# Kernel optimization log

Measured on AMD Instinct MI355X. Metric: run time of the kernel, lower is better.

The kernel has to match this reference:

```python
import jax, jax.numpy as jnp
import numpy as np
import math

B = 512          # graphs per batch
NP = 200         # nodes per graph
E_PER = 2000     # edges per graph
V = 50000        # item vocab
EMB = 9
HID = 128
RATIO = 0.8
K1 = math.ceil(RATIO * NP)   # 160
K2 = math.ceil(RATIO * K1)   # 128
K3 = math.ceil(RATIO * K2)   # 103


def sage_conv(x, src, dst, valid, n, w_neigh, w_root, b):
    # PyG SAGEConv: lin_l(mean_{j->i} x_j) + lin_r(x_i) + bias
    msg = x[src] * valid[:, None]                      # [E, C]
    seg = jnp.where(valid > 0, dst, n)                 # invalid edges -> dummy segment
    s = jax.ops.segment_sum(msg, seg, num_segments=n + 1)[:n]
    cnt = jax.ops.segment_sum(valid, seg, num_segments=n + 1)[:n]
    mean = s / jnp.maximum(cnt, 1.0)[:, None]
    return mean @ w_neigh.T + x @ w_root.T + b


def topk_pool(x, src, dst, valid, np_cur, k, p):
    # TopKPooling: score = tanh(x.p/||p||); keep top-k per graph; x *= score
    n = x.shape[0]
    score = jnp.tanh((x @ p) / jnp.linalg.norm(p))
    topv, topi = jax.lax.top_k(score.reshape(B, np_cur), k)   # [B, k]
    kept = (jnp.arange(B)[:, None] * np_cur + topi).reshape(-1)
    n_new = B * k
    x_new = x[kept] * topv.reshape(-1)[:, None]
    mapping = jnp.full((n,), -1, dtype=jnp.int32).at[kept].set(
        jnp.arange(n_new, dtype=jnp.int32))
    ns, nd = mapping[src], mapping[dst]
    valid_new = valid * ((ns >= 0) & (nd >= 0)).astype(valid.dtype)
    return x_new, jnp.maximum(ns, 0), jnp.maximum(nd, 0), valid_new


def global_pool(x, k):
    # cat([global_max_pool, global_mean_pool]) with uniform graph size k
    xr = x.reshape(B, k, -1)
    return jnp.concatenate([xr.max(axis=1), xr.mean(axis=1)], axis=1)


def setup_inputs() -> dict:
    key = jax.random.key(0)
    ks = jax.random.split(key, 24)
    # block-structured intra-graph edges
    s = jax.random.randint(ks[0], (B, E_PER), 0, NP)
    d = jax.random.randint(ks[1], (B, E_PER), 0, NP)
    off = (jnp.arange(B) * NP)[:, None]
    edge_index = jnp.stack([(s + off).reshape(-1), (d + off).reshape(-1)]).astype(jnp.int32)
    node_ids = jax.random.randint(ks[2], (B * NP, 1), 0, V)
    batch = jnp.repeat(jnp.arange(B), NP)
    sc = 0.1
    p = {
        'emb': jax.random.normal(ks[3], (V, EMB)) * sc,
        'w1n': jax.random.normal(ks[4], (HID, EMB)) * sc,
        'w1r': jax.random.normal(ks[5], (HID, EMB)) * sc,
        'b1': jnp.zeros((HID,)),
        'w2n': jax.random.normal(ks[6], (HID, HID)) * sc,
        'w2r': jax.random.normal(ks[7], (HID, HID)) * sc,
        'b2': jnp.zeros((HID,)),
        'w3n': jax.random.normal(ks[8], (HID, HID)) * sc,
        'w3r': jax.random.normal(ks[9], (HID, HID)) * sc,
        'b3': jnp.zeros((HID,)),
        'p1': jax.random.normal(ks[10], (HID,)) * sc,
        'p2': jax.random.normal(ks[11], (HID,)) * sc,
        'p3': jax.random.normal(ks[12], (HID,)) * sc,
        'lw1': jax.random.normal(ks[13], (HID, 2 * HID)) * sc,
        'lb1': jnp.zeros((HID,)),
        'lw2': jax.random.normal(ks[14], (64, HID)) * sc,
        'lb2': jnp.zeros((64,)),
        'lw3': jax.random.normal(ks[15], (1, 64)) * sc,
        'lb3': jnp.zeros((1,)),
    }
    return {'node_ids': node_ids, 'edge_index': edge_index, 'batch': batch, **p}


def reference(node_ids, edge_index, batch, emb, w1n, w1r, b1, w2n, w2r, b2,
              w3n, w3r, b3, p1, p2, p3, lw1, lb1, lw2, lb2, lw3, lb3):
    src, dst = edge_index[0], edge_index[1]
    valid = jnp.ones(src.shape[0], dtype=jnp.float32)
    x = emb[node_ids[:, 0]]                                  # [N, 9]
    x = jax.nn.relu(sage_conv(x, src, dst, valid, B * NP, w1n, w1r, b1))
    x, src, dst, valid = topk_pool(x, src, dst, valid, NP, K1, p1)
    x1 = global_pool(x, K1)
    x = jax.nn.relu(sage_conv(x, src, dst, valid, B * K1, w2n, w2r, b2))
    x, src, dst, valid = topk_pool(x, src, dst, valid, K1, K2, p2)
    x2 = global_pool(x, K2)
    x = jax.nn.relu(sage_conv(x, src, dst, valid, B * K2, w3n, w3r, b3))
    x, src, dst, valid = topk_pool(x, src, dst, valid, K2, K3, p3)
    x3 = global_pool(x, K3)
    h = x1 + x2 + x3                                         # [B, 256]
    h = jax.nn.relu(h @ lw1.T + lb1)
    h = jax.nn.relu(h @ lw2.T + lb2)
    return jax.nn.sigmoid(h @ lw3.T + lb3)[:, 0]             # [B]
```

## Files before the change

kernel.cpp:

```cpp
#include <hip/hip_runtime.h>
#include <math.h>

constexpr int B    = 512;
constexpr int NPG  = 200;
constexpr int EPER = 2000;
constexpr int EMB  = 9;
constexpr int HID  = 128;
constexpr int K1   = 160;
constexpr int K2   = 128;
constexpr int K3   = 103;
constexpr int N0   = B * NPG;
constexpr int N1   = B * K1;
constexpr int N2   = B * K2;
constexpr int E    = B * EPER;

__global__ __launch_bounds__(256) void k_stage1(
        const int* __restrict__ node_ids,
        const float* __restrict__ emb,
        const int* __restrict__ es, const int* __restrict__ ed,
        const float* __restrict__ w1n, const float* __restrict__ w1r,
        const float* __restrict__ b1, const float* __restrict__ p1,
        float* __restrict__ xout,
        int* __restrict__ mapping,
        float* __restrict__ gout) {
    const int g = blockIdx.x, tid = threadIdx.x;
    __shared__ float x0L[NPG * EMB];
    __shared__ float mnL[NPG * EMB];
    __shared__ int   idsL[NPG];
    __shared__ int   deg[256];
    __shared__ int   off2[257];
    __shared__ int   cur[256];
    __shared__ int   csr[EPER];
    __shared__ float sc[NPG];
    __shared__ int   pos[NPG];
    __shared__ float redM[4 * 128], redS[4 * 128];

    if (tid < NPG) idsL[tid] = node_ids[g * NPG + tid];
    deg[tid] = 0;
    __syncthreads();
    for (int i = tid; i < NPG * EMB; i += 256) {
        int n = i / EMB, j = i - n * EMB;
        x0L[i] = emb[(size_t)idsL[n] * EMB + j];
    }
    const int ebase = g * EPER, nbase = g * NPG;
    int lsrc[8], ldst[8];
    #pragma unroll
    for (int q = 0; q < 8; q++) {
        int e = tid + q * 256;
        lsrc[q] = es[ebase + e] - nbase;
        ldst[q] = ed[ebase + e] - nbase;
        atomicAdd(&deg[ldst[q]], 1);
    }
    __syncthreads();
    cur[tid] = deg[tid];
    __syncthreads();
    #pragma unroll
    for (int d = 1; d < 256; d <<= 1) {
        int t = (tid >= d) ? cur[tid - d] : 0;
        __syncthreads();
        cur[tid] += t;
        __syncthreads();
    }
    if (tid == 0) off2[0] = 0;
    off2[tid + 1] = cur[tid];
    __syncthreads();
    cur[tid] = off2[tid];
    __syncthreads();
    #pragma unroll
    for (int q = 0; q < 8; q++) {
        int slot = atomicAdd(&cur[ldst[q]], 1);
        csr[slot] = lsrc[q];
    }
    __syncthreads();
    if (tid < NPG) {
        int bg = off2[tid], en = off2[tid + 1];
        float a[EMB];
        #pragma unroll
        for (int j = 0; j < EMB; j++) a[j] = 0.f;
        for (int t = bg; t < en; t++) {
            int s = csr[t];
            #pragma unroll
            for (int j = 0; j < EMB; j++) a[j] += x0L[s * EMB + j];
        }
        float inv = 1.f / (float)((en - bg) > 1 ? (en - bg) : 1);
        #pragma unroll
        for (int j = 0; j < EMB; j++) mnL[tid * EMB + j] = a[j] * inv;
    }
    const int lane = tid & 63, wv = tid >> 6;
    float pl0 = p1[lane], pl1 = p1[64 + lane];
    float pp = pl0 * pl0 + pl1 * pl1;
    #pragma unroll
    for (int o = 32; o >= 1; o >>= 1) pp += __shfl_xor(pp, o, 64);
    float nrm = sqrtf(pp);
    float wn0[EMB], wn1[EMB], wr0[EMB], wr1[EMB];
    #pragma unroll
    for (int j = 0; j < EMB; j++) {
        wn0[j] = w1n[lane * EMB + j];
        wn1[j] = w1n[(lane + 64) * EMB + j];
        wr0[j] = w1r[lane * EMB + j];
        wr1[j] = w1r[(lane + 64) * EMB + j];
    }
    float bb0 = b1[lane], bb1 = b1[64 + lane];
    __syncthreads();
    for (int i = wv; i < NPG; i += 4) {
        float c0 = bb0, c1 = bb1;
        #pragma unroll
        for (int j = 0; j < EMB; j++) {
            float m = mnL[i * EMB + j];
            float x = x0L[i * EMB + j];
            c0 += m * wn0[j] + x * wr0[j];
            c1 += m * wn1[j] + x * wr1[j];
        }
        c0 = fmaxf(c0, 0.f);
        c1 = fmaxf(c1, 0.f);
        float d = c0 * pl0 + c1 * pl1;
        #pragma unroll
        for (int o = 32; o >= 1; o >>= 1) d += __shfl_xor(d, o, 64);
        if (lane == 0) sc[i] = tanhf(d / nrm);
    }
    __syncthreads();
    if (tid < NPG) {
        float scv = sc[tid];
        int rank = 0;
        for (int j = 0; j < NPG; j++) {
            float o = sc[j];
            rank += (o > scv) || (o == scv && j < tid);
        }
        bool keep = rank < K1;
        pos[tid] = keep ? rank : -1;
        mapping[g * NPG + tid] = keep ? (g * K1 + rank) : -1;
    }
    __syncthreads();
    float pm0 = -INFINITY, pm1 = -INFINITY, ps0 = 0.f, ps1 = 0.f;
    for (int i = wv; i < NPG; i += 4) {
        int r = pos[i];
        if (r < 0) continue;
        float c0 = bb0, c1 = bb1;
        #pragma unroll
        for (int j = 0; j < EMB; j++) {
            float m = mnL[i * EMB + j];
            float x = x0L[i * EMB + j];
            c0 += m * wn0[j] + x * wr0[j];
            c1 += m * wn1[j] + x * wr1[j];
        }
        float s = sc[i];
        float v0 = fmaxf(c0, 0.f) * s;
        float v1 = fmaxf(c1, 0.f) * s;
        long rowp = (long)(g * K1 + r) * HID;
        xout[rowp + lane] = v0;
        xout[rowp + 64 + lane] = v1;
        pm0 = fmaxf(pm0, v0); ps0 += v0;
        pm1 = fmaxf(pm1, v1); ps1 += v1;
    }
    redM[wv * 128 + lane] = pm0;      redS[wv * 128 + lane] = ps0;
    redM[wv * 128 + 64 + lane] = pm1; redS[wv * 128 + 64 + lane] = ps1;
    __syncthreads();
    if (tid < 128) {
        float mx = redM[tid], sm = redS[tid];
        #pragma unroll
        for (int w2 = 1; w2 < 4; w2++) {
            mx = fmaxf(mx, redM[w2 * 128 + tid]);
            sm += redS[w2 * 128 + tid];
        }
        gout[g * 256 + tid] = mx;
        gout[g * 256 + 128 + tid] = sm / (float)K1;
    }
}

template <int MROWS, int KKEEP, int NTHR, int MINW>
__global__ __launch_bounds__(NTHR, MINW) void k_stage23(
        const float* __restrict__ xin,
        const int* __restrict__ es, const int* __restrict__ ed,
        const int* __restrict__ map1,
        const int* __restrict__ map2,
        const float* __restrict__ wn, const float* __restrict__ wr,
        const float* __restrict__ bb, const float* __restrict__ p,
        float* __restrict__ xout,
        int* __restrict__ mapout,
        float* __restrict__ gout) {
    constexpr int TRM = MROWS / 8;
    __shared__ float xY[MROWS * 132];
    __shared__ float Bw[2 * 32 * 132];
    __shared__ int   csr[EPER];
    __shared__ int   deg[256], scanb[256], off2[257], cur[256];
    __shared__ float sc[MROWS];
    __shared__ int   pos[MROWS];
    __shared__ float nrmL;

    const int tid = threadIdx.x;
    const int g = blockIdx.x;
    const long row0 = (long)g * MROWS;
    const int tc = tid & 31, tr = tid >> 5;

    for (int i = tid; i < MROWS * 32; i += NTHR) {
        int r = i >> 5, c = (i & 31) * 4;
        *(float4*)&xY[r * 132 + c] =
            *(const float4*)(xin + (row0 + r) * HID + c);
    }
    if (tid < 256) deg[tid] = 0;
    __syncthreads();
    const int ebase = g * EPER, nbase = g * MROWS;
    for (int e = tid; e < EPER; e += NTHR) {
        int a = map1[es[ebase + e]];
        int b = map1[ed[ebase + e]];
        if (map2) {
            a = (a >= 0) ? map2[a] : -1;
            b = (b >= 0) ? map2[b] : -1;
        }
        if (a >= 0 && b >= 0) atomicAdd(&deg[b - nbase], 1);
    }
    __syncthreads();
    if (tid < 256) scanb[tid] = deg[tid];
    __syncthreads();
    #pragma unroll
    for (int d = 1; d < 256; d <<= 1) {
        int t = (tid < 256 && tid >= d) ? scanb[tid - d] : 0;
        __syncthreads();
        if (tid < 256) scanb[tid] += t;
        __syncthreads();
    }
    if (tid == 0) off2[0] = 0;
    if (tid < 256) off2[tid + 1] = scanb[tid];
    __syncthreads();
    if (tid < 256) cur[tid] = off2[tid];
    __syncthreads();
    for (int e = tid; e < EPER; e += NTHR) {
        int a = map1[es[ebase + e]];
        int b = map1[ed[ebase + e]];
        if (map2) {
            a = (a >= 0) ? map2[a] : -1;
            b = (b >= 0) ? map2[b] : -1;
        }
        if (a >= 0 && b >= 0) {
            int slot = atomicAdd(&cur[b - nbase], 1);
            csr[slot] = a - nbase;
        }
    }
    if (tid < 64) {
        float a = p[tid], b2 = p[64 + tid];
        float pp = a * a + b2 * b2;
        #pragma unroll
        for (int o = 32; o >= 1; o >>= 1) pp += __shfl_xor(pp, o, 64);
        if (tid == 0) nrmL = sqrtf(pp);
    }
    __syncthreads();

    float accY[8][4], accZ[8][4];
    #pragma unroll
    for (int r = 0; r < 8; r++)
        #pragma unroll
        for (int c = 0; c < 4; c++) { accY[r][c] = 0.f; accZ[r][c] = 0.f; }

    const int sr = tid >> 3, sc4 = (tid & 7) * 4;
    const bool stager = (sr < 64);
    const float* wsrc0 = (sr < 32) ? wn : wr;
    const int wrow = (sr < 32) ? sr : sr - 32;
    float* Bmine = Bw + ((sr < 32) ? 0 : 32 * 132);
    float4 bvv[4];
    if (stager) {
        #pragma unroll
        for (int i = 0; i < 4; i++)
            bvv[i] = *(const float4*)(wsrc0 + (size_t)(wrow + i * 32) * HID + sc4);
    }
    for (int ch = 0; ch < 4; ch++) {
        if (stager) {
            #pragma unroll
            for (int i = 0; i < 4; i++) {
                int r = wrow + i * 32;
                Bmine[(sc4 + 0) * 132 + r] = bvv[i].x;
                Bmine[(sc4 + 1) * 132 + r] = bvv[i].y;
                Bmine[(sc4 + 2) * 132 + r] = bvv[i].z;
                Bmine[(sc4 + 3) * 132 + r] = bvv[i].w;
            }
        }
        __syncthreads();
        if (ch + 1 < 4 && stager) {
            #pragma unroll
            for (int i = 0; i < 4; i++)
                bvv[i] = *(const float4*)(wsrc0 + (size_t)(wrow + i * 32) * HID
                                          + (ch + 1) * 32 + sc4);
        }
        for (int kq = 0; kq < 8; kq++) {
            float4 af[8];
            #pragma unroll
            for (int rr = 0; rr < 8; rr++)
                af[rr] = *(const float4*)&xY[(tr * 8 + rr) * 132 + ch * 32 + kq * 4];
            #pragma unroll
            for (int kk = 0; kk < 4; kk++) {
                int k = kq * 4 + kk;
                float4 bn = *(const float4*)&Bw[k * 132 + tc * 4];
                float4 br = *(const float4*)&Bw[32 * 132 + k * 132 + tc * 4];
                #pragma unroll
                for (int rr = 0; rr < 8; rr++) {
                    float a = (kk == 0) ? af[rr].x : (kk == 1) ? af[rr].y
                             : (kk == 2) ? af[rr].z : af[rr].w;
                    accY[rr][0] += a * bn.x; accY[rr][1] += a * bn.y;
                    accY[rr][2] += a * bn.z; accY[rr][3] += a * bn.w;
                    accZ[rr][0] += a * br.x; accZ[rr][1] += a * br.y;
                    accZ[rr][2] += a * br.z; accZ[rr][3] += a * br.w;
                }
            }
        }
        __syncthreads();
    }

    #pragma unroll
    for (int rr = 0; rr < 8; rr++) {
        float4 yv = {accY[rr][0], accY[rr][1], accY[rr][2], accY[rr][3]};
        *(float4*)&xY[(tr * 8 + rr) * 132 + tc * 4] = yv;
    }
    __syncthreads();

    float bias[4], pv[4];
    #pragma unroll
    for (int c = 0; c < 4; c++) {
        bias[c] = bb[tc * 4 + c];
        pv[c]   = p[tc * 4 + c];
    }
    float outv[8][4];
    #pragma unroll
    for (int rr = 0; rr < 8; rr++) {
        int m = tr * 8 + rr;
        int bg = off2[m], en = off2[m + 1];
        float s0 = 0.f, s1 = 0.f, s2 = 0.f, s3 = 0.f;
        for (int t = bg; t < en; t++) {
            float4 yv = *(const float4*)&xY[csr[t] * 132 + tc * 4];
            s0 += yv.x; s1 += yv.y; s2 += yv.z; s3 += yv.w;
        }
        float inv = 1.f / (float)((en - bg) > 1 ? (en - bg) : 1);
        outv[rr][0] = fmaxf(s0 * inv + accZ[rr][0] + bias[0], 0.f);
        outv[rr][1] = fmaxf(s1 * inv + accZ[rr][1] + bias[1], 0.f);
        outv[rr][2] = fmaxf(s2 * inv + accZ[rr][2] + bias[2], 0.f);
        outv[rr][3] = fmaxf(s3 * inv + accZ[rr][3] + bias[3], 0.f);
    }

    float* scpart = Bw;
    #pragma unroll
    for (int rr = 0; rr < 8; rr++) {
        float sp = outv[rr][0] * pv[0] + outv[rr][1] * pv[1]
                 + outv[rr][2] * pv[2] + outv[rr][3] * pv[3];
        scpart[(tr * 8 + rr) * 32 + tc] = sp;
    }
    __syncthreads();
    if (tid < MROWS) {
        float sum = 0.f;
        #pragma unroll
        for (int t = 0; t < 32; t++) sum += scpart[tid * 32 + t];
        sc[tid] = tanhf(sum / nrmL);
    }
    __syncthreads();
    if (tid < MROWS) {
        float scv = sc[tid];
        int rank = 0;
        for (int j = 0; j < MROWS; j++) {
            float o = sc[j];
            rank += (o > scv) || (o == scv && j < tid);
        }
        bool keep = rank < KKEEP;
        pos[tid] = keep ? rank : -1;
        if (mapout) mapout[g * MROWS + tid] = keep ? (g * KKEEP + rank) : -1;
    }
    __syncthreads();
    float cm[4], cs[4];
    #pragma unroll
    for (int c = 0; c < 4; c++) { cm[c] = -INFINITY; cs[c] = 0.f; }
    #pragma unroll
    for (int rr = 0; rr < 8; rr++) {
        int m = tr * 8 + rr;
        int r = pos[m];
        if (r < 0) continue;
        float sv = sc[m];
        float v0 = outv[rr][0] * sv, v1 = outv[rr][1] * sv;
        float v2 = outv[rr][2] * sv, v3 = outv[rr][3] * sv;
        cm[0] = fmaxf(cm[0], v0); cs[0] += v0;
        cm[1] = fmaxf(cm[1], v1); cs[1] += v1;
        cm[2] = fmaxf(cm[2], v2); cs[2] += v2;
        cm[3] = fmaxf(cm[3], v3); cs[3] += v3;
        if (xout) {
            float4 o0 = {v0, v1, v2, v3};
            *(float4*)(xout + ((long)g * KKEEP + r) * HID + tc * 4) = o0;
        }
    }
    float* redM = Bw;
    float* redS = Bw + TRM * 128;
    #pragma unroll
    for (int c = 0; c < 4; c++) {
        redM[tr * 128 + tc * 4 + c] = cm[c];
        redS[tr * 128 + tc * 4 + c] = cs[c];
    }
    __syncthreads();
    if (tid < 128) {
        float mx = redM[tid], sm = redS[tid];
        #pragma unroll 4
        for (int t = 1; t < TRM; t++) {
            mx = fmaxf(mx, redM[t * 128 + tid]);
            sm += redS[t * 128 + tid];
        }
        gout[g * 256 + tid] = mx;
        gout[g * 256 + 128 + tid] = sm / (float)KKEEP;
    }
}

__global__ __launch_bounds__(128) void k_mlp(const float* __restrict__ g1, const float* __restrict__ g2,
                      const float* __restrict__ g3,
                      const float* __restrict__ lw1, const float* __restrict__ lb1,
                      const float* __restrict__ lw2, const float* __restrict__ lb2,
                      const float* __restrict__ lw3, const float* __restrict__ lb3,
                      float* __restrict__ out) {
    int g = blockIdx.x, t = threadIdx.x;
    __shared__ float h0[256];
    __shared__ float h1[128];
    __shared__ float h2r[64];
    h0[t]       = g1[g * 256 + t] + g2[g * 256 + t] + g3[g * 256 + t];
    h0[t + 128] = g1[g * 256 + 128 + t] + g2[g * 256 + 128 + t] + g3[g * 256 + 128 + t];
    __syncthreads();
    float a = lb1[t];
    #pragma unroll 4
    for (int j = 0; j < 256; j++) a += h0[j] * lw1[t * 256 + j];
    h1[t] = fmaxf(a, 0.f);
    __syncthreads();
    if (t < 64) {
        float a2 = lb2[t];
        #pragma unroll 4
        for (int j = 0; j < 128; j++) a2 += h1[j] * lw2[t * 128 + j];
        h2r[t] = fmaxf(a2, 0.f) * lw3[t];
    }
    __syncthreads();
    if (t == 0) {
        float s = 0.f;
        for (int j = 0; j < 64; j++) s += h2r[j];
        s += lb3[0];
        out[g] = 1.f / (1.f + expf(-s));
    }
}

extern "C" void kernel_launch(void* const* d_in, const int* in_sizes, int n_in,
                              void* d_out, int out_size, void* d_ws, size_t ws_size,
                              hipStream_t stream) {
    const int*   node_ids = (const int*)d_in[0];
    const int*   ei   = (const int*)d_in[1];
    const float* emb  = (const float*)d_in[3];
    const float* w1n  = (const float*)d_in[4];
    const float* w1r  = (const float*)d_in[5];
    const float* b1   = (const float*)d_in[6];
    const float* w2n  = (const float*)d_in[7];
    const float* w2r  = (const float*)d_in[8];
    const float* b2   = (const float*)d_in[9];
    const float* w3n  = (const float*)d_in[10];
    const float* w3r  = (const float*)d_in[11];
    const float* b3   = (const float*)d_in[12];
    const float* p1   = (const float*)d_in[13];
    const float* p2   = (const float*)d_in[14];
    const float* p3   = (const float*)d_in[15];
    const float* lw1  = (const float*)d_in[16];
    const float* lb1  = (const float*)d_in[17];
    const float* lw2  = (const float*)d_in[18];
    const float* lb2  = (const float*)d_in[19];
    const float* lw3  = (const float*)d_in[20];
    const float* lb3  = (const float*)d_in[21];
    float* out = (float*)d_out;

    float* ws  = (float*)d_ws;
    float* D   = ws;
    float* D2  = D + (size_t)N1 * HID;
    float* g1  = D2 + (size_t)N2 * HID;
    float* g2  = g1 + B * 2 * HID;
    float* g3  = g2 + B * 2 * HID;
    int* map1  = (int*)(g3 + B * 2 * HID);
    int* map2  = map1 + N0;

    k_stage1<<<B, 256, 0, stream>>>(node_ids, emb, ei, ei + E,
                                    w1n, w1r, b1, p1, D, map1, g1);

    k_stage23<K1, K2, 640, 3><<<B, 640, 0, stream>>>(
        D, ei, ei + E, map1, nullptr, w2n, w2r, b2, p2, D2, map2, g2);

    k_stage23<K2, K3, 512, 2><<<B, 512, 0, stream>>>(
        D2, ei, ei + E, map1, map2, w3n, w3r, b3, p3, nullptr, nullptr, g3);

    k_mlp<<<B, 128, 0, stream>>>(g1, g2, g3, lw1, lb1, lw2, lb2, lw3, lb3, out);
}
```

Measured before the change: 379.1 us.

## Fuse all three conv/pool stages into one per-graph kernel

Merges stage1 and both stage2/3 kernels into a single 640-thread block per graph that keeps pooled node features in shared memory between stages. Edge remapping uses local shared-memory position arrays instead of global mapping tables. This removes the global write and re-read of the intermediate feature matrices and mapping arrays, plus two kernel launches. In exchange it uses a larger shared-memory footprint and runs stage 1 with a 640-thread block, which may limit occupancy.

```diff
diff --git a/kernel.cpp b/kernel.cpp
--- a/kernel.cpp
+++ b/kernel.cpp
@@ -9,395 +9,555 @@
 constexpr int K1   = 160;
 constexpr int K2   = 128;
 constexpr int K3   = 103;
-constexpr int N0   = B * NPG;
-constexpr int N1   = B * K1;
-constexpr int N2   = B * K2;
 constexpr int E    = B * EPER;
 
-__global__ __launch_bounds__(256) void k_stage1(
+__global__ __launch_bounds__(640, 2) void k_fused(
         const int* __restrict__ node_ids,
         const float* __restrict__ emb,
         const int* __restrict__ es, const int* __restrict__ ed,
         const float* __restrict__ w1n, const float* __restrict__ w1r,
         const float* __restrict__ b1, const float* __restrict__ p1,
-        float* __restrict__ xout,
-        int* __restrict__ mapping,
-        float* __restrict__ gout) {
+        const float* __restrict__ w2n, const float* __restrict__ w2r,
+        const float* __restrict__ b2, const float* __restrict__ p2,
+        const float* __restrict__ w3n, const float* __restrict__ w3r,
+        const float* __restrict__ b3, const float* __restrict__ p3,
+        float* __restrict__ g1, float* __restrict__ g2,
+        float* __restrict__ g3) {
     const int g = blockIdx.x, tid = threadIdx.x;
-    __shared__ float x0L[NPG * EMB];
-    __shared__ float mnL[NPG * EMB];
-    __shared__ int   idsL[NPG];
-    __shared__ int   deg[256];
-    __shared__ int   off2[257];
-    __shared__ int   cur[256];
-    __shared__ int   csr[EPER];
-    __shared__ float sc[NPG];
-    __shared__ int   pos[NPG];
-    __shared__ float redM[4 * 128], redS[4 * 128];
-
-    if (tid < NPG) idsL[tid] = node_ids[g * NPG + tid];
-    deg[tid] = 0;
-    __syncthreads();
-    for (int i = tid; i < NPG * EMB; i += 256) {
-        int n = i / EMB, j = i - n * EMB;
-        x0L[i] = emb[(size_t)idsL[n] * EMB + j];
-    }
-    const int ebase = g * EPER, nbase = g * NPG;
-    int lsrc[8], ldst[8];
-    #pragma unroll
-    for (int q = 0; q < 8; q++) {
-        int e = tid + q * 256;
-        lsrc[q] = es[ebase + e] - nbase;
-        ldst[q] = ed[ebase + e] - nbase;
-        atomicAdd(&deg[ldst[q]], 1);
-    }
-    __syncthreads();
-    cur[tid] = deg[tid];
-    __syncthreads();
-    #pragma unroll
-    for (int d = 1; d < 256; d <<= 1) {
-        int t = (tid >= d) ? cur[tid - d] : 0;
-        __syncthreads();
-        cur[tid] += t;
-        __syncthreads();
-    }
-    if (tid == 0) off2[0] = 0;
-    off2[tid + 1] = cur[tid];
-    __syncthreads();
-    cur[tid] = off2[tid];
-    __syncthreads();
-    #pragma unroll
-    for (int q = 0; q < 8; q++) {
-        int slot = atomicAdd(&cur[ldst[q]], 1);
-        csr[slot] = lsrc[q];
-    }
-    __syncthreads();
-    if (tid < NPG) {
-        int bg = off2[tid], en = off2[tid + 1];
-        float a[EMB];
-        #pragma unroll
-        for (int j = 0; j < EMB; j++) a[j] = 0.f;
-        for (int t = bg; t < en; t++) {
-            int s = csr[t];
-            #pragma unroll
-            for (int j = 0; j < EMB; j++) a[j] += x0L[s * EMB + j];
-        }
-        float inv = 1.f / (float)((en - bg) > 1 ? (en - bg) : 1);
-        #pragma unroll
-        for (int j = 0; j < EMB; j++) mnL[tid * EMB + j] = a[j] * inv;
-    }
     const int lane = tid & 63, wv = tid >> 6;
-    float pl0 = p1[lane], pl1 = p1[64 + lane];
-    float pp = pl0 * pl0 + pl1 * pl1;
-    #pragma unroll
-    for (int o = 32; o >= 1; o >>= 1) pp += __shfl_xor(pp, o, 64);
-    float nrm = sqrtf(pp);
-    float wn0[EMB], wn1[EMB], wr0[EMB], wr1[EMB];
-    #pragma unroll
-    for (int j = 0; j < EMB; j++) {
-        wn0[j] = w1n[lane * EMB + j];
-        wn1[j] = w1n[(lane + 64) * EMB + j];
-        wr0[j] = w1r[lane * EMB + j];
-        wr1[j] = w1r[(lane + 64) * EMB + j];
-    }
-    float bb0 = b1[lane], bb1 = b1[64 + lane];
-    __syncthreads();
-    for (int i = wv; i < NPG; i += 4) {
-        float c0 = bb0, c1 = bb1;
-        #pragma unroll
-        for (int j = 0; j < EMB; j++) {
-            float m = mnL[i * EMB + j];
-            float x = x0L[i * EMB + j];
-            c0 += m * wn0[j] + x * wr0[j];
-            c1 += m * wn1[j] + x * wr1[j];
-        }
-        c0 = fmaxf(c0, 0.f);
-        c1 = fmaxf(c1, 0.f);
-        float d = c0 * pl0 + c1 * pl1;
-        #pragma unroll
-        for (int o = 32; o >= 1; o >>= 1) d += __shfl_xor(d, o, 64);
-        if (lane == 0) sc[i] = tanhf(d / nrm);
-    }
-    __syncthreads();
-    if (tid < NPG) {
-        float scv = sc[tid];
-        int rank = 0;
-        for (int j = 0; j < NPG; j++) {
-            float o = sc[j];
-            rank += (o > scv) || (o == scv && j < tid);
-        }
-        bool keep = rank < K1;
-        pos[tid] = keep ? rank : -1;
-        mapping[g * NPG + tid] = keep ? (g * K1 + rank) : -1;
-    }
-    __syncthreads();
-    float pm0 = -INFINITY, pm1 = -INFINITY, ps0 = 0.f, ps1 = 0.f;
-    for (int i = wv; i < NPG; i += 4) {
-        int r = pos[i];
-        if (r < 0) continue;
-        float c0 = bb0, c1 = bb1;
-        #pragma unroll
-        for (int j = 0; j < EMB; j++) {
-            float m = mnL[i * EMB + j];
-            float x = x0L[i * EMB + j];
-            c0 += m * wn0[j] + x * wr0[j];
-            c1 += m * wn1[j] + x * wr1[j];
-        }
-        float s = sc[i];
-        float v0 = fmaxf(c0, 0.f) * s;
-        float v1 = fmaxf(c1, 0.f) * s;
-        long rowp = (long)(g * K1 + r) * HID;
-        xout[rowp + lane] = v0;
-        xout[rowp + 64 + lane] = v1;
-        pm0 = fmaxf(pm0, v0); ps0 += v0;
-        pm1 = fmaxf(pm1, v1); ps1 += v1;
-    }
-    redM[wv * 128 + lane] = pm0;      redS[wv * 128 + lane] = ps0;
-    redM[wv * 128 + 64 + lane] = pm1; redS[wv * 128 + 64 + lane] = ps1;
-    __syncthreads();
-    if (tid < 128) {
-        float mx = redM[tid], sm = redS[tid];
-        #pragma unroll
-        for (int w2 = 1; w2 < 4; w2++) {
-            mx = fmaxf(mx, redM[w2 * 128 + tid]);
-            sm += redS[w2 * 128 + tid];
-        }
-        gout[g * 256 + tid] = mx;
-        gout[g * 256 + 128 + tid] = sm / (float)K1;
-    }
-}
-
-template <int MROWS, int KKEEP, int NTHR, int MINW>
-__global__ __launch_bounds__(NTHR, MINW) void k_stage23(
-        const float* __restrict__ xin,
-        const int* __restrict__ es, const int* __restrict__ ed,
-        const int* __restrict__ map1,
-        const int* __restrict__ map2,
-        const float* __restrict__ wn, const float* __restrict__ wr,
-        const float* __restrict__ bb, const float* __restrict__ p,
-        float* __restrict__ xout,
-        int* __restrict__ mapout,
-        float* __restrict__ gout) {
-    constexpr int TRM = MROWS / 8;
-    __shared__ float xY[MROWS * 132];
-    __shared__ float Bw[2 * 32 * 132];
+
+    __shared__ float xY[K1 * 132];
+    __shared__ float S[2 * 32 * 132];
     __shared__ int   csr[EPER];
     __shared__ int   deg[256], scanb[256], off2[257], cur[256];
-    __shared__ float sc[MROWS];
-    __shared__ int   pos[MROWS];
-    __shared__ float nrmL;
-
-    const int tid = threadIdx.x;
-    const int g = blockIdx.x;
-    const long row0 = (long)g * MROWS;
-    const int tc = tid & 31, tr = tid >> 5;
-
-    for (int i = tid; i < MROWS * 32; i += NTHR) {
-        int r = i >> 5, c = (i & 31) * 4;
-        *(float4*)&xY[r * 132 + c] =
-            *(const float4*)(xin + (row0 + r) * HID + c);
+    __shared__ int   idsL[NPG];
+    __shared__ float sc[NPG];
+    __shared__ int   pos1[NPG], pos2[K1];
+
+    const int eb = g * EPER, nb0 = g * NPG;
+
+    {
+        float* x0L  = S;
+        float* mnL  = S + 1800;
+        float* redA = S + 3600;
+        if (tid < NPG) idsL[tid] = node_ids[g * NPG + tid];
+        if (tid < 256) deg[tid] = 0;
+        __syncthreads();
+        for (int i = tid; i < NPG * EMB; i += 640) {
+            int n = i / EMB, j = i - n * EMB;
+            x0L[i] = emb[(size_t)idsL[n] * EMB + j];
+        }
+        for (int e = tid; e < EPER; e += 640)
+            atomicAdd(&deg[ed[eb + e] - nb0], 1);
+        __syncthreads();
+        if (tid < 256) scanb[tid] = deg[tid];
+        __syncthreads();
+        #pragma unroll
+        for (int d = 1; d < 256; d <<= 1) {
+            int t = (tid < 256 && tid >= d) ? scanb[tid - d] : 0;
+            __syncthreads();
+            if (tid < 256) scanb[tid] += t;
+            __syncthreads();
+        }
+        if (tid == 0) off2[0] = 0;
+        if (tid < 256) off2[tid + 1] = scanb[tid];
+        __syncthreads();
+        if (tid < 256) cur[tid] = off2[tid];
+        __syncthreads();
+        for (int e = tid; e < EPER; e += 640) {
+            int slot = atomicAdd(&cur[ed[eb + e] - nb0], 1);
+            csr[slot] = es[eb + e] - nb0;
+        }
+        __syncthreads();
+        if (tid < NPG) {
+            int bg = off2[tid], en = off2[tid + 1];
+            float a[EMB];
+            #pragma unroll
+            for (int j = 0; j < EMB; j++) a[j] = 0.f;
+            for (int t = bg; t < en; t++) {
+                int s = csr[t];
+                #pragma unroll
+                for (int j = 0; j < EMB; j++) a[j] += x0L[s * EMB + j];
+            }
+            float inv = 1.f / (float)((en - bg) > 1 ? (en - bg) : 1);
+            #pragma unroll
+            for (int j = 0; j < EMB; j++) mnL[tid * EMB + j] = a[j] * inv;
+        }
+        float pl0 = p1[lane], pl1 = p1[64 + lane];
+        float pp = pl0 * pl0 + pl1 * pl1;
+        #pragma unroll
+        for (int o = 32; o >= 1; o >>= 1) pp += __shfl_xor(pp, o, 64);
+        float nrm = sqrtf(pp);
+        float wn0[EMB], wn1[EMB], wr0[EMB], wr1[EMB];
+        #pragma unroll
+        for (int j = 0; j < EMB; j++) {
+            wn0[j] = w1n[lane * EMB + j];
+            wn1[j] = w1n[(lane + 64) * EMB + j];
+            wr0[j] = w1r[lane * EMB + j];
+            wr1[j] = w1r[(lane + 64) * EMB + j];
+        }
+        float bb0 = b1[lane], bb1 = b1[64 + lane];
+        __syncthreads();
+        for (int i = wv; i < NPG; i += 10) {
+            float c0 = bb0, c1 = bb1;
+            #pragma unroll
+            for (int j = 0; j < EMB; j++) {
+                float m = mnL[i * EMB + j];
+                float x = x0L[i * EMB + j];
+                c0 += m * wn0[j] + x * wr0[j];
+                c1 += m * wn1[j] + x * wr1[j];
+            }
+            c0 = fmaxf(c0, 0.f);
+            c1 = fmaxf(c1, 0.f);
+            float d = c0 * pl0 + c1 * pl1;
+            #pragma unroll
+            for (int o = 32; o >= 1; o >>= 1) d += __shfl_xor(d, o, 64);
+            if (lane == 0) sc[i] = tanhf(d / nrm);
+        }
+        __syncthreads();
+        if (tid < NPG) {
+            float scv = sc[tid];
+            int rank = 0;
+            for (int j = 0; j < NPG; j++) {
+                float o = sc[j];
+                rank += (o > scv) || (o == scv && j < tid);
+            }
+            pos1[tid] = (rank < K1) ? rank : -1;
+        }
+        __syncthreads();
+        float pm0 = -INFINITY, pm1 = -INFINITY, ps0 = 0.f, ps1 = 0.f;
+        for (int i = wv; i < NPG; i += 10) {
+            int r = pos1[i];
+            if (r < 0) continue;
+            float c0 = bb0, c1 = bb1;
+            #pragma unroll
+            for (int j = 0; j < EMB; j++) {
+                float m = mnL[i * EMB + j];
+                float x = x0L[i * EMB + j];
+                c0 += m * wn0[j] + x * wr0[j];
+                c1 += m * wn1[j] + x * wr1[j];
+            }
+            float s = sc[i];
+            float v0 = fmaxf(c0, 0.f) * s;
+            float v1 = fmaxf(c1, 0.f) * s;
+            xY[r * 132 + lane] = v0;
+            xY[r * 132 + 64 + lane] = v1;
+            pm0 = fmaxf(pm0, v0); ps0 += v0;
+            pm1 = fmaxf(pm1, v1); ps1 += v1;
+        }
+        redA[wv * 128 + lane] = pm0;
+        redA[wv * 128 + 64 + lane] = pm1;
+        redA[1280 + wv * 128 + lane] = ps0;
+        redA[1280 + wv * 128 + 64 + lane] = ps1;
+        __syncthreads();
+        if (tid < 128) {
+            float mx = redA[tid], sm = redA[1280 + tid];
+            #pragma unroll
+            for (int w = 1; w < 10; w++) {
+                mx = fmaxf(mx, redA[w * 128 + tid]);
+                sm += redA[1280 + w * 128 + tid];
+            }
+            g1[g * 256 + tid] = mx;
+            g1[g * 256 + 128 + tid] = sm / (float)K1;
+        }
+        __syncthreads();
     }
-    if (tid < 256) deg[tid] = 0;
-    __syncthreads();
-    const int ebase = g * EPER, nbase = g * MROWS;
-    for (int e = tid; e < EPER; e += NTHR) {
-        int a = map1[es[ebase + e]];
-        int b = map1[ed[ebase + e]];
-        if (map2) {
-            a = (a >= 0) ? map2[a] : -1;
-            b = (b >= 0) ? map2[b] : -1;
-        }
-        if (a >= 0 && b >= 0) atomicAdd(&deg[b - nbase], 1);
+
+    {
+        if (tid < 256) deg[tid] = 0;
+        __syncthreads();
+        for (int e = tid; e < EPER; e += 640) {
+            int a = pos1[es[eb + e] - nb0];
+            int b = pos1[ed[eb + e] - nb0];
+            if (a >= 0 && b >= 0) atomicAdd(&deg[b], 1);
+        }
+        __syncthreads();
+        if (tid < 256) scanb[tid] = deg[tid];
+        __syncthreads();
+        #pragma unroll
+        for (int d = 1; d < 256; d <<= 1) {
+            int t = (tid < 256 && tid >= d) ? scanb[tid - d] : 0;
+            __syncthreads();
+            if (tid < 256) scanb[tid] += t;
+            __syncthreads();
+        }
+        if (tid == 0) off2[0] = 0;
+        if (tid < 256) off2[tid + 1] = scanb[tid];
+        __syncthreads();
+        if (tid < 256) cur[tid] = off2[tid];
+        __syncthreads();
+        for (int e = tid; e < EPER; e += 640) {
+            int a = pos1[es[eb + e] - nb0];
+            int b = pos1[ed[eb + e] - nb0];
+            if (a >= 0 && b >= 0) {
+                int slot = atomicAdd(&cur[b], 1);
+                csr[slot] = a;
+            }
+        }
+        __syncthreads();
+
+        const int tc = tid & 31, tr = tid >> 5;
+        float accY[8][4], accZ[8][4];
+        #pragma unroll
+        for (int r = 0; r < 8; r++)
+            #pragma unroll
+            for (int c = 0; c < 4; c++) { accY[r][c] = 0.f; accZ[r][c] = 0.f; }
+
+        const int sr = tid >> 3, sc4 = (tid & 7) * 4;
+        const bool stager = (sr < 64);
+        const float* wsrc0 = (sr < 32) ? w2n : w2r;
+        const int wrow = (sr < 32) ? sr : sr - 32;
+        float* Bmine = S + ((sr < 32) ? 0 : 32 * 132);
+        float4 bvv[4];
+        if (stager) {
+            #pragma unroll
+            for (int i = 0; i < 4; i++)
+                bvv[i] = *(const float4*)(wsrc0 + (size_t)(wrow + i * 32) * HID + sc4);
+        }
+        for (int ch = 0; ch < 4; ch++) {
+            if (stager) {
+                #pragma unroll
+                for (int i = 0; i < 4; i++) {
+                    int r = wrow + i * 32;
+                    Bmine[(sc4 + 0) * 132 + r] = bvv[i].x;
+                    Bmine[(sc4 + 1) * 132 + r] = bvv[i].y;
+                    Bmine[(sc4 + 2) * 132 + r] = bvv[i].z;
+                    Bmine[(sc4 + 3) * 132 + r] = bvv[i].w;
+                }
+            }
+            __syncthreads();
+            if (ch + 1 < 4 && stager) {
+                #pragma unroll
+                for (int i = 0; i < 4; i++)
+                    bvv[i] = *(const float4*)(wsrc0 + (size_t)(wrow + i * 32) * HID
+                                              + (ch + 1) * 32 + sc4);
+            }
+            for (int kq = 0; kq < 8; kq++) {
+                float4 af[8];
+                #pragma unroll
+                for (int rr = 0; rr < 8; rr++)
+                    af[rr] = *(const float4*)&xY[(tr * 8 + rr) * 132 + ch * 32 + kq * 4];
+                #pragma unroll
+                for (int kk = 0; kk < 4; kk++) {
+                    int k = kq * 4 + kk;
+                    float4 bn = *(const float4*)&S[k * 132 + tc * 4];
+                    float4 br = *(const float4*)&S[32 * 132 + k * 132 + tc * 4];
+                    #pragma unroll
+                    for (int rr = 0; rr < 8; rr++) {
+                        float a = (kk == 0) ? af[rr].x : (kk == 1) ? af[rr].y
+                                 : (kk == 2) ? af[rr].z : af[rr].w;
+                        accY[rr][0] += a * bn.x; accY[rr][1] += a * bn.y;
+                        accY[rr][2] += a * bn.z; accY[rr][3] += a * bn.w;
+                        accZ[rr][0] += a * br.x; accZ[rr][1] += a * br.y;
+                        accZ[rr][2] += a * br.z; accZ[rr][3] += a * br.w;
+                    }
+                }
+            }
+            __syncthreads();
+        }
+        #pragma unroll
+        for (int rr = 0; rr < 8; rr++) {
+            float4 yv = {accY[rr][0], accY[rr][1], accY[rr][2], accY[rr][3]};
+            *(float4*)&xY[(tr * 8 + rr) * 132 + tc * 4] = yv;
+        }
+        __syncthreads();
+
+        float bias[4], pv[4];
+        #pragma unroll
+        for (int c = 0; c < 4; c++) {
+            bias[c] = b2[tc * 4 + c];
+            pv[c]   = p2[tc * 4 + c];
+        }
+        float a0 = p2[lane], a1 = p2[64 + lane];
+        float pp = a0 * a0 + a1 * a1;
+        #pragma unroll
+        for (int o = 32; o >= 1; o >>= 1) pp += __shfl_xor(pp, o, 64);
+        float nrm = sqrtf(pp);
+        float outv[8][4];
+        #pragma unroll
+        for (int rr = 0; rr < 8; rr++) {
+            int m = tr * 8 + rr;
+            int bg = off2[m], en = off2[m + 1];
+            float s0 = 0.f, s1 = 0.f, s2 = 0.f, s3 = 0.f;
+            for (int t = bg; t < en; t++) {
+                float4 yv = *(const float4*)&xY[csr[t] * 132 + tc * 4];
+                s0 += yv.x; s1 += yv.y; s2 += yv.z; s3 += yv.w;
+            }
+            float inv = 1.f / (float)((en - bg) > 1 ? (en - bg) : 1);
+            outv[rr][0] = fmaxf(s0 * inv + accZ[rr][0] + bias[0], 0.f);
+            outv[rr][1] = fmaxf(s1 * inv + accZ[rr][1] + bias[1], 0.f);
+            outv[rr][2] = fmaxf(s2 * inv + accZ[rr][2] + bias[2], 0.f);
+            outv[rr][3] = fmaxf(s3 * inv + accZ[rr][3] + bias[3], 0.f);
+        }
+        float* scpart = S;
+        __syncthreads();
+        #pragma unroll
+        for (int rr = 0; rr < 8; rr++) {
+            float sp = outv[rr][0] * pv[0] + outv[rr][1] * pv[1]
+                     + outv[rr][2] * pv[2] + outv[rr][3] * pv[3];
+            scpart[(tr * 8 + rr) * 32 + tc] = sp;
+        }
+        __syncthreads();
+        if (tid < K1) {
+            float sum = 0.f;
+            #pragma unroll
+            for (int t = 0; t < 32; t++) sum += scpart[tid * 32 + t];
+            sc[tid] = tanhf(sum / nrm);
+        }
+        __syncthreads();
+        if (tid < K1) {
+            float scv = sc[tid];
+            int rank = 0;
+            for (int j = 0; j < K1; j++) {
+                float o = sc[j];
+                rank += (o > scv) || (o == scv && j < tid);
+            }
+            pos2[tid] = (rank < K2) ? rank : -1;
+        }
+        __syncthreads();
+        float cm[4], cs[4];
+        #pragma unroll
+        for (int c = 0; c < 4; c++) { cm[c] = -INFINITY; cs[c] = 0.f; }
+        #pragma unroll
+        for (int rr = 0; rr < 8; rr++) {
+            int m = tr * 8 + rr;
+            int r = pos2[m];
+            if (r < 0) continue;
+            float sv = sc[m];
+            float v0 = outv[rr][0] * sv, v1 = outv[rr][1] * sv;
+            float v2 = outv[rr][2] * sv, v3 = outv[rr][3] * sv;
+            cm[0] = fmaxf(cm[0], v0); cs[0] += v0;
+            cm[1] = fmaxf(cm[1], v1); cs[1] += v1;
+            cm[2] = fmaxf(cm[2], v2); cs[2] += v2;
+            cm[3] = fmaxf(cm[3], v3); cs[3] += v3;
+            float4 o0 = {v0, v1, v2, v3};
+            *(float4*)&xY[r * 132 + tc * 4] = o0;
+        }
+        float* redM = S;
+        float* redS = S + 20 * 128;
+        #pragma unroll
+        for (int c = 0; c < 4; c++) {
+            redM[tr * 128 + tc * 4 + c] = cm[c];
+            redS[tr * 128 + tc * 4 + c] = cs[c];
+        }
+        __syncthreads();
+        if (tid < 128) {
+            float mx = redM[tid], sm = redS[tid];
+            #pragma unroll 4
+            for (int t = 1; t < 20; t++) {
+                mx = fmaxf(mx, redM[t * 128 + tid]);
+                sm += redS[t * 128 + tid];
+            }
+            g2[g * 256 + tid] = mx;
+            g2[g * 256 + 128 + tid] = sm / (float)K2;
+        }
+        __syncthreads();
     }
-    __syncthreads();
-    if (tid < 256) scanb[tid] = deg[tid];
-    __syncthreads();
-    #pragma unroll
-    for (int d = 1; d < 256; d <<= 1) {
-        int t = (tid < 256 && tid >= d) ? scanb[tid - d] : 0;
-        __syncthreads();
-        if (tid < 256) scanb[tid] += t;
-        __syncthreads();
-    }
-    if (tid == 0) off2[0] = 0;
-    if (tid < 256) off2[tid + 1] = scanb[tid];
-    __syncthreads();
-    if (tid < 256) cur[tid] = off2[tid];
-    __syncthreads();
-    for (int e = tid; e < EPER; e += NTHR) {
-        int a = map1[es[ebase + e]];
-        int b = map1[ed[ebase + e]];
-        if (map2) {
-            a = (a >= 0) ? map2[a] : -1;
-            b = (b >= 0) ? map2[b] : -1;
-        }
-        if (a >= 0 && b >= 0) {
-            int slot = atomicAdd(&cur[b - nbase], 1);
-            csr[slot] = a - nbase;
-        }
-    }
-    if (tid < 64) {
-        float a = p[tid], b2 = p[64 + tid];
-        float pp = a * a + b2 * b2;
+
+    {
+        if (tid < 256) deg[tid] = 0;
+        __syncthreads();
+        for (int e = tid; e < EPER; e += 640) {
+            int a = pos1[es[eb + e] - nb0];
+            int b = pos1[ed[eb + e] - nb0];
+            a = (a >= 0) ? pos2[a] : -1;
+            b = (b >= 0) ? pos2[b] : -1;
+            if (a >= 0 && b >= 0) atomicAdd(&deg[b], 1);
+        }
+        __syncthreads();
+        if (tid < 256) scanb[tid] = deg[tid];
+        __syncthreads();
+        #pragma unroll
+        for (int d = 1; d < 256; d <<= 1) {
+            int t = (tid < 256 && tid >= d) ? scanb[tid - d] : 0;
+            __syncthreads();
+            if (tid < 256) scanb[tid] += t;
+            __syncthreads();
+        }
+        if (tid == 0) off2[0] = 0;
+        if (tid < 256) off2[tid + 1] = scanb[tid];
+        __syncthreads();
+        if (tid < 256) cur[tid] = off2[tid];
+        __syncthreads();
+        for (int e = tid; e < EPER; e += 640) {
+            int a = pos1[es[eb + e] - nb0];
+            int b = pos1[ed[eb + e] - nb0];
+            a = (a >= 0) ? pos2[a] : -1;
+            b = (b >= 0) ? pos2[b] : -1;
+            if (a >= 0 && b >= 0) {
+                int slot = atomicAdd(&cur[b], 1);
+                csr[slot] = a;
+            }
+        }
+        __syncthreads();
+
+        const int tc = tid & 31, tr = tid >> 5;
+        const bool comp = (tid < 512);
+        float accY[8][4], accZ[8][4];
+        #pragma unroll
+        for (int r = 0; r < 8; r++)
+            #pragma unroll
+            for (int c = 0; c < 4; c++) { accY[r][c] = 0.f; accZ[r][c] = 0.f; }
+
+        const int sr = tid >> 3, sc4 = (tid & 7) * 4;
+        const bool stager = (sr < 64);
+        const float* wsrc0 = (sr < 32) ? w3n : w3r;
+        const int wrow = (sr < 32) ? sr : sr - 32;
+        float* Bmine = S + ((sr < 32) ? 0 : 32 * 132);
+        float4 bvv[4];
+        if (stager) {
+            #pragma unroll
+            for (int i = 0; i < 4; i++)
+                bvv[i] = *(const float4*)(wsrc0 + (size_t)(wrow + i * 32) * HID + sc4);
+        }
+        for (int ch = 0; ch < 4; ch++) {
+            if (stager) {
+                #pragma unroll
+                for (int i = 0; i < 4; i++) {
+                    int r = wrow + i * 32;
+                    Bmine[(sc4 + 0) * 132 + r] = bvv[i].x;
+                    Bmine[(sc4 + 1) * 132 + r] = bvv[i].y;
+                    Bmine[(sc4 + 2) * 132 + r] = bvv[i].z;
+                    Bmine[(sc4 + 3) * 132 + r] = bvv[i].w;
+                }
+            }
+            __syncthreads();
+            if (ch + 1 < 4 && stager) {
+                #pragma unroll
+                for (int i = 0; i < 4; i++)
+                    bvv[i] = *(const float4*)(wsrc0 + (size_t)(wrow + i * 32) * HID
+                                              + (ch + 1) * 32 + sc4);
+            }
+            if (comp) {
+                for (int kq = 0; kq < 8; kq++) {
+                    float4 af[8];
+                    #pragma unroll
+                    for (int rr = 0; rr < 8; rr++)
+                        af[rr] = *(const float4*)&xY[(tr * 8 + rr) * 132 + ch * 32 + kq * 4];
+                    #pragma unroll
+                    for (int kk = 0; kk < 4; kk++) {
+                        int k = kq * 4 + kk;
+                        float4 bn = *(const float4*)&S[k * 132 + tc * 4];
+                        float4 br = *(const float4*)&S[32 * 132 + k * 132 + tc * 4];
+                        #pragma unroll
+                        for (int rr = 0; rr < 8; rr++) {
+                            float a = (kk == 0) ? af[rr].x : (kk == 1) ? af[rr].y
+                                     : (kk == 2) ? af[rr].z : af[rr].w;
+                            accY[rr][0] += a * bn.x; accY[rr][1] += a * bn.y;
+                            accY[rr][2] += a * bn.z; accY[rr][3] += a * bn.w;
+                            accZ[rr][0] += a * br.x; accZ[rr][1] += a * br.y;
+                            accZ[rr][2] += a * br.z; accZ[rr][3] += a * br.w;
+                        }
+                    }
+                }
+            }
+            __syncthreads();
+        }
+        if (comp) {
+            #pragma unroll
+            for (int rr = 0; rr < 8; rr++) {
+                float4 yv = {accY[rr][0], accY[rr][1], accY[rr][2], accY[rr][3]};
+                *(float4*)&xY[(tr * 8 + rr) * 132 + tc * 4] = yv;
+            }
+        }
+        __syncthreads();
+
+        float bias[4], pv[4];
+        #pragma unroll
+        for (int c = 0; c < 4; c++) {
+            bias[c] = b3[tc * 4 + c];
+            pv[c]   = p3[tc * 4 + c];
+        }
+        float a0 = p3[lane], a1 = p3[64 + lane];
+        float pp = a0 * a0 + a1 * a1;
         #pragma unroll
         for (int o = 32; o >= 1; o >>= 1) pp += __shfl_xor(pp, o, 64);
-        if (tid == 0) nrmL = sqrtf(pp);
-    }
-    __syncthreads();
-
-    float accY[8][4], accZ[8][4];
-    #pragma unroll
-    for (int r = 0; r < 8; r++)
-        #pragma unroll
-        for (int c = 0; c < 4; c++) { accY[r][c] = 0.f; accZ[r][c] = 0.f; }
-
-    const int sr = tid >> 3, sc4 = (tid & 7) * 4;
-    const bool stager = (sr < 64);
-    const float* wsrc0 = (sr < 32) ? wn : wr;
-    const int wrow = (sr < 32) ? sr : sr - 32;
-    float* Bmine = Bw + ((sr < 32) ? 0 : 32 * 132);
-    float4 bvv[4];
-    if (stager) {
-        #pragma unroll
-        for (int i = 0; i < 4; i++)
-            bvv[i] = *(const float4*)(wsrc0 + (size_t)(wrow + i * 32) * HID + sc4);
-    }
-    for (int ch = 0; ch < 4; ch++) {
-        if (stager) {
-            #pragma unroll
-            for (int i = 0; i < 4; i++) {
-                int r = wrow + i * 32;
-                Bmine[(sc4 + 0) * 132 + r] = bvv[i].x;
-                Bmine[(sc4 + 1) * 132 + r] = bvv[i].y;
-                Bmine[(sc4 + 2) * 132 + r] = bvv[i].z;
-                Bmine[(sc4 + 3) * 132 + r] = bvv[i].w;
-            }
-        }
-        __syncthreads();
-        if (ch + 1 < 4 && stager) {
-            #pragma unroll
-            for (int i = 0; i < 4; i++)
-                bvv[i] = *(const float4*)(wsrc0 + (size_t)(wrow + i * 32) * HID
-                                          + (ch + 1) * 32 + sc4);
-        }
-        for (int kq = 0; kq < 8; kq++) {
-            float4 af[8];
-            #pragma unroll
-            for (int rr = 0; rr < 8; rr++)
-                af[rr] = *(const float4*)&xY[(tr * 8 + rr) * 132 + ch * 32 + kq * 4];
-            #pragma unroll
-            for (int kk = 0; kk < 4; kk++) {
-                int k = kq * 4 + kk;
-                float4 bn = *(const float4*)&Bw[k * 132 + tc * 4];
-                float4 br = *(const float4*)&Bw[32 * 132 + k * 132 + tc * 4];
-                #pragma unroll
-                for (int rr = 0; rr < 8; rr++) {
-                    float a = (kk == 0) ? af[rr].x : (kk == 1) ? af[rr].y
-                             : (kk == 2) ? af[rr].z : af[rr].w;
-                    accY[rr][0] += a * bn.x; accY[rr][1] += a * bn.y;
-                    accY[rr][2] += a * bn.z; accY[rr][3] += a * bn.w;
-                    accZ[rr][0] += a * br.x; accZ[rr][1] += a * br.y;
-                    accZ[rr][2] += a * br.z; accZ[rr][3] += a * br.w;
+        float nrm = sqrtf(pp);
+        float outv[8][4];
+        float* scpart = S;
+        if (comp) {
+            #pragma unroll
+            for (int rr = 0; rr < 8; rr++) {
+                int m = tr * 8 + rr;
+                int bg = off2[m], en = off2[m + 1];
+                float s0 = 0.f, s1 = 0.f, s2 = 0.f, s3 = 0.f;
+                for (int t = bg; t < en; t++) {
+                    float4 yv = *(const float4*)&xY[csr[t] * 132 + tc * 4];
+                    s0 += yv.x; s1 += yv.y; s2 += yv.z; s3 += yv.w;
                 }
-            }
-        }
-        __syncthreads();
-    }
-
-    #pragma unroll
-    for (int rr = 0; rr < 8; rr++) {
-        float4 yv = {accY[rr][0], accY[rr][1], accY[rr][2], accY[rr][3]};
-        *(float4*)&xY[(tr * 8 + rr) * 132 + tc * 4] = yv;
-    }
-    __syncthreads();
-
-    float bias[4], pv[4];
-    #pragma unroll
-    for (int c = 0; c < 4; c++) {
-        bias[c] = bb[tc * 4 + c];
-        pv[c]   = p[tc * 4 + c];
-    }
-    float outv[8][4];
-    #pragma unroll
-    for (int rr = 0; rr < 8; rr++) {
-        int m = tr * 8 + rr;
-        int bg = off2[m], en = off2[m + 1];
-        float s0 = 0.f, s1 = 0.f, s2 = 0.f, s3 = 0.f;
-        for (int t = bg; t < en; t++) {
-            float4 yv = *(const float4*)&xY[csr[t] * 132 + tc * 4];
-            s0 += yv.x; s1 += yv.y; s2 += yv.z; s3 += yv.w;
-        }
-        float inv = 1.f / (float)((en - bg) > 1 ? (en - bg) : 1);
-        outv[rr][0] = fmaxf(s0 * inv + accZ[rr][0] + bias[0], 0.f);
-        outv[rr][1] = fmaxf(s1 * inv + accZ[rr][1] + bias[1], 0.f);
-        outv[rr][2] = fmaxf(s2 * inv + accZ[rr][2] + bias[2], 0.f);
-        outv[rr][3] = fmaxf(s3 * inv + accZ[rr][3] + bias[3], 0.f);
-    }
-
-    float* scpart = Bw;
-    #pragma unroll
-    for (int rr = 0; rr < 8; rr++) {
-        float sp = outv[rr][0] * pv[0] + outv[rr][1] * pv[1]
-                 + outv[rr][2] * pv[2] + outv[rr][3] * pv[3];
-        scpart[(tr * 8 + rr) * 32 + tc] = sp;
-    }
-    __syncthreads();
-    if (tid < MROWS) {
-        float sum = 0.f;
-        #pragma unroll
-        for (int t = 0; t < 32; t++) sum += scpart[tid * 32 + t];
-        sc[tid] = tanhf(sum / nrmL);
-    }
-    __syncthreads();
-    if (tid < MROWS) {
-        float scv = sc[tid];
-        int rank = 0;
-        for (int j = 0; j < MROWS; j++) {
-            float o = sc[j];
-            rank += (o > scv) || (o == scv && j < tid);
-        }
-        bool keep = rank < KKEEP;
-        pos[tid] = keep ? rank : -1;
-        if (mapout) mapout[g * MROWS + tid] = keep ? (g * KKEEP + rank) : -1;
-    }
-    __syncthreads();
-    float cm[4], cs[4];
-    #pragma unroll
-    for (int c = 0; c < 4; c++) { cm[c] = -INFINITY; cs[c] = 0.f; }
-    #pragma unroll
-    for (int rr = 0; rr < 8; rr++) {
-        int m = tr * 8 + rr;
-        int r = pos[m];
-        if (r < 0) continue;
-        float sv = sc[m];
-        float v0 = outv[rr][0] * sv, v1 = outv[rr][1] * sv;
-        float v2 = outv[rr][2] * sv, v3 = outv[rr][3] * sv;
-        cm[0] = fmaxf(cm[0], v0); cs[0] += v0;
-        cm[1] = fmaxf(cm[1], v1); cs[1] += v1;
-        cm[2] = fmaxf(cm[2], v2); cs[2] += v2;
-        cm[3] = fmaxf(cm[3], v3); cs[3] += v3;
-        if (xout) {
-            float4 o0 = {v0, v1, v2, v3};
-            *(float4*)(xout + ((long)g * KKEEP + r) * HID + tc * 4) = o0;
-        }
-    }
-    float* redM = Bw;
-    float* redS = Bw + TRM * 128;
-    #pragma unroll
-    for (int c = 0; c < 4; c++) {
-        redM[tr * 128 + tc * 4 + c] = cm[c];
-        redS[tr * 128 + tc * 4 + c] = cs[c];
-    }
-    __syncthreads();
-    if (tid < 128) {
-        float mx = redM[tid], sm = redS[tid];
-        #pragma unroll 4
-        for (int t = 1; t < TRM; t++) {
-            mx = fmaxf(mx, redM[t * 128 + tid]);
-            sm += redS[t * 128 + tid];
-        }
-        gout[g * 256 + tid] = mx;
-        gout[g * 256 + 128 + tid] = sm / (float)KKEEP;
+                float inv = 1.f / (float)((en - bg) > 1 ? (en - bg) : 1);
+                outv[rr][0] = fmaxf(s0 * inv + accZ[rr][0] + bias[0], 0.f);
+                outv[rr][1] = fmaxf(s1 * inv + accZ[rr][1] + bias[1], 0.f);
+                outv[rr][2] = fmaxf(s2 * inv + accZ[rr][2] + bias[2], 0.f);
+                outv[rr][3] = fmaxf(s3 * inv + accZ[rr][3] + bias[3], 0.f);
+            }
+        }
+        __syncthreads();
+        if (comp) {
+            #pragma unroll
+            for (int rr = 0; rr < 8; rr++) {
+                float sp = outv[rr][0] * pv[0] + outv[rr][1] * pv[1]
+                         + outv[rr][2] * pv[2] + outv[rr][3] * pv[3];
+                scpart[(tr * 8 + rr) * 32 + tc] = sp;
+            }
+        }
+        __syncthreads();
+        if (tid < K2) {
+            float sum = 0.f;
+            #pragma unroll
+            for (int t = 0; t < 32; t++) sum += scpart[tid * 32 + t];
+            sc[tid] = tanhf(sum / nrm);
+        }
+        __syncthreads();
+        int* posC = idsL;
+        if (tid < K2) {
+            float scv = sc[tid];
+            int rank = 0;
+            for (int j = 0; j < K2; j++) {
+                float o = sc[j];
+                rank += (o > scv) || (o == scv && j < tid);
+            }
+            posC[tid] = (rank < K3) ? rank : -1;
+        }
+        __syncthreads();
+        float cm[4], cs[4];
+        #pragma unroll
+        for (int c = 0; c < 4; c++) { cm[c] = -INFINITY; cs[c] = 0.f; }
+        if (comp) {
+            #pragma unroll
+            for (int rr = 0; rr < 8; rr++) {
+                int m = tr * 8 + rr;
+                int r = posC[m];
+                if (r < 0) continue;
+                float sv = sc[m];
+                #pragma unroll
+                for (int c = 0; c < 4; c++) {
+                    float v = outv[rr][c] * sv;
+                    cm[c] = fmaxf(cm[c], v);
+                    cs[c] += v;
+                }
+            }
+        }
+        float* redM = S;
+        float* redS = S + 16 * 128;
+        if (comp) {
+            #pragma unroll
+            for (int c = 0; c < 4; c++) {
+                redM[tr * 128 + tc * 4 + c] = cm[c];
+                redS[tr * 128 + tc * 4 + c] = cs[c];
+            }
+        }
+        __syncthreads();
+        if (tid < 128) {
+            float mx = redM[tid], sm = redS[tid];
+            #pragma unroll 4
+            for (int t = 1; t < 16; t++) {
+                mx = fmaxf(mx, redM[t * 128 + tid]);
+                sm += redS[t * 128 + tid];
+            }
+            g3[g * 256 + tid] = mx;
+            g3[g * 256 + 128 + tid] = sm / (float)K3;
+        }
     }
 }
 
@@ -461,22 +621,14 @@
     float* out = (float*)d_out;
 
     float* ws  = (float*)d_ws;
-    float* D   = ws;
-    float* D2  = D + (size_t)N1 * HID;
-    float* g1  = D2 + (size_t)N2 * HID;
+    float* g1  = ws;
     float* g2  = g1 + B * 2 * HID;
     float* g3  = g2 + B * 2 * HID;
-    int* map1  = (int*)(g3 + B * 2 * HID);
-    int* map2  = map1 + N0;
-
-    k_stage1<<<B, 256, 0, stream>>>(node_ids, emb, ei, ei + E,
-                                    w1n, w1r, b1, p1, D, map1, g1);
-
-    k_stage23<K1, K2, 640, 3><<<B, 640, 0, stream>>>(
-        D, ei, ei + E, map1, nullptr, w2n, w2r, b2, p2, D2, map2, g2);
-
-    k_stage23<K2, K3, 512, 2><<<B, 512, 0, stream>>>(
-        D2, ei, ei + E, map1, map2, w3n, w3r, b3, p3, nullptr, nullptr, g3);
-
+
+    k_fused<<<B, 640, 0, stream>>>(node_ids, emb, ei, ei + E,
+                                   w1n, w1r, b1, p1,
+                                   w2n, w2r, b2, p2,
+                                   w3n, w3r, b3, p3,
+                                   g1, g2, g3);
     k_mlp<<<B, 128, 0, stream>>>(g1, g2, g3, lw1, lb1, lw2, lb2, lw3, lb3, out);
 }
```

Measured after the change: 364.3 us. -3.9%, faster.
